# Kernel tuning notes

Measured on AMD Instinct MI355X. Metric: run time of the kernel, lower is better.

The kernel has to match this reference:

```python
import jax, jax.numpy as jnp
import numpy as np

N = 50000
IN_DIM = 128
HID = 16
HEADS = 8
NUM_CLASSES = 16
NEG_SLOPE = 0.2


def _glorot(key, shape):
    fan_in, fan_out = shape[0], shape[-1]
    lim = float(np.sqrt(6.0 / (fan_in + fan_out)))
    return jax.random.uniform(key, shape, jnp.float32, -lim, lim)


def setup_inputs() -> dict:
    key = jax.random.key(0)
    ks = jax.random.split(key, 12)
    x = jax.random.normal(ks[0], (N, IN_DIM), jnp.float32)
    edge_index = jax.random.randint(ks[1], (2, 1600000), 0, N, jnp.int64)
    # conv1: in=IN_DIM, out per head=HID, heads=HEADS
    Wl1 = _glorot(ks[2], (IN_DIM, HEADS * HID))
    Wr1 = _glorot(ks[3], (IN_DIM, HEADS * HID))
    att1 = _glorot(ks[4], (HEADS, HID))
    b1 = jnp.zeros((HEADS * HID,), jnp.float32)
    # conv2: in=HID*HEADS, out per head=NUM_CLASSES
    Wl2 = _glorot(ks[5], (HEADS * HID, HEADS * NUM_CLASSES))
    Wr2 = _glorot(ks[6], (HEADS * HID, HEADS * NUM_CLASSES))
    att2 = _glorot(ks[7], (HEADS, NUM_CLASSES))
    b2 = jnp.zeros((HEADS * NUM_CLASSES,), jnp.float32)
    # final linear: NUM_CLASSES*HEADS -> NUM_CLASSES
    Wlin = _glorot(ks[8], (HEADS * NUM_CLASSES, NUM_CLASSES))
    blin = jnp.zeros((NUM_CLASSES,), jnp.float32)
    return dict(x=x, edge_index=edge_index, Wl1=Wl1, Wr1=Wr1, att1=att1, b1=b1,
                Wl2=Wl2, Wr2=Wr2, att2=att2, b2=b2, Wlin=Wlin, blin=blin)


def _gatv2_conv(x, src, dst, Wl, Wr, att, bias, heads, out_ch):
    n = x.shape[0]
    xl = (x @ Wl).reshape(n, heads, out_ch)  # source transform
    xr = (x @ Wr).reshape(n, heads, out_ch)  # target transform
    # additive attention logits per edge (GATv2)
    e = jax.nn.leaky_relu(xl[src] + xr[dst], NEG_SLOPE)          # [E,H,C]
    logits = jnp.einsum('ehc,hc->eh', e, att)                     # [E,H]
    # per-destination segment softmax
    m = jax.ops.segment_max(logits, dst, num_segments=n)          # [N,H]
    a = jnp.exp(logits - m[dst])                                  # [E,H]
    s = jax.ops.segment_sum(a, dst, num_segments=n)               # [N,H]
    alpha = a / (s[dst] + 1e-16)
    out = jax.ops.segment_sum(alpha[:, :, None] * xl[src], dst, num_segments=n)
    return out.reshape(n, heads * out_ch) + bias


def reference(x, edge_index, Wl1, Wr1, att1, b1, Wl2, Wr2, att2, b2, Wlin, blin):
    n = x.shape[0]
    # add self-loops (PyG GATv2Conv default add_self_loops=True)
    loop = jnp.arange(n, dtype=edge_index.dtype)
    src = jnp.concatenate([edge_index[0], loop])
    dst = jnp.concatenate([edge_index[1], loop])
    h = _gatv2_conv(x, src, dst, Wl1, Wr1, att1, b1, HEADS, HID)
    h = jax.nn.relu(h)  # dropout identity in eval mode
    h = _gatv2_conv(h, src, dst, Wl2, Wr2, att2, b2, HEADS, NUM_CLASSES)
    h = jax.nn.relu(h)
    logits = h @ Wlin + blin
    return jax.nn.log_softmax(logits, axis=1)
```

## Files before the change

kernel.cpp:

```cpp
#include <hip/hip_runtime.h>

#define HEADS 8
#define FDIM 128
#define NCLS 16
#define NEG_SLOPE 0.2f
#define LOG2E 1.4426950408889634f

typedef __attribute__((ext_vector_type(8))) short bf16x8;
typedef __attribute__((ext_vector_type(4))) float f32x4;

__device__ __forceinline__ unsigned short f2bf(float f) {
    unsigned u = __float_as_uint(f);
    unsigned r = u + 0x7FFFu + ((u >> 16) & 1u);
    return (unsigned short)(r >> 16);
}

__global__ __launch_bounds__(256) void gemm_csr(const float* __restrict__ Xf,
                                                const unsigned short* __restrict__ Xb,
                                                const float* __restrict__ W0,
                                                const float* __restrict__ W1,
                                                unsigned short* __restrict__ Y0,
                                                unsigned short* __restrict__ Y1,
                                                int n,
                                                const int* __restrict__ srcs,
                                                const int* __restrict__ dsts,
                                                int* __restrict__ cnt,
                                                int* __restrict__ adj,
                                                int E0, int pad, int GB, int SB) {
    __shared__ __align__(16) unsigned short ws[8 * 4 * 64 * 8];
    const int t = threadIdx.x;
    const int x = blockIdx.x;
    if (x >= 2 * GB) {
        int i = (x - 2 * GB) * 256 + t;
        const int stride = SB * 256;
        for (; i < E0; i += stride) {
            const int d = dsts[i];
            const int rk = atomicAdd(&cnt[d], 1);
            if (rk < pad) adj[(size_t)d * pad + rk] = srcs[i];
        }
        return;
    }
    const int side = (x >= GB) ? 1 : 0;
    const float* W = side ? W1 : W0;
    unsigned short* Y = side ? Y1 : Y0;

#pragma unroll
    for (int i = 0; i < 16; i++) {
        const int f = t + i * 256;
        const int k = f >> 5, n4 = f & 31;
        const float4 v = *(const float4*)(W + k * 128 + n4 * 4);
        const int kc = k >> 5, q = (k >> 3) & 3, j = k & 7;
        const float vv[4] = {v.x, v.y, v.z, v.w};
#pragma unroll
        for (int e = 0; e < 4; e++) {
            const int nn = n4 * 4 + e;
            ws[((((nn >> 4) * 4 + kc) * 64 + q * 16 + (nn & 15)) << 3) + j] = f2bf(vv[e]);
        }
    }
    __syncthreads();

    const int w = t >> 6, lane = t & 63;
    const int q = lane >> 4, m = lane & 15;
    const bf16x8* wb = (const bf16x8*)ws;
    const int Gh = (n + 63) >> 6;
    const int bid = side ? x - GB : x;

    for (int tile = bid; tile < Gh; tile += GB) {
        const int nb = tile * 64;
        const int arow = nb + w * 16 + m;
        bf16x8 af[4];
        if (arow < n) {
            if (Xb) {
                const unsigned short* xp = Xb + (size_t)arow * 128 + q * 8;
#pragma unroll
                for (int kc = 0; kc < 4; kc++) af[kc] = *(const bf16x8*)(xp + kc * 32);
            } else {
                const float* xp = Xf + (size_t)arow * 128 + q * 8;
#pragma unroll
                for (int kc = 0; kc < 4; kc++) {
                    const float4 v0 = *(const float4*)(xp + kc * 32);
                    const float4 v1 = *(const float4*)(xp + kc * 32 + 4);
                    union { unsigned short us[8]; bf16x8 b; } pk;
                    pk.us[0] = f2bf(v0.x); pk.us[1] = f2bf(v0.y);
                    pk.us[2] = f2bf(v0.z); pk.us[3] = f2bf(v0.w);
                    pk.us[4] = f2bf(v1.x); pk.us[5] = f2bf(v1.y);
                    pk.us[6] = f2bf(v1.z); pk.us[7] = f2bf(v1.w);
                    af[kc] = pk.b;
                }
            }
        } else {
#pragma unroll
            for (int kc = 0; kc < 4; kc++) af[kc] = (bf16x8){0,0,0,0,0,0,0,0};
        }
        f32x4 acc[8];
#pragma unroll
        for (int i = 0; i < 8; i++) acc[i] = (f32x4){0.f, 0.f, 0.f, 0.f};
#pragma unroll
        for (int kc = 0; kc < 4; kc++) {
#pragma unroll
            for (int ct = 0; ct < 8; ct++)
                acc[ct] = __builtin_amdgcn_mfma_f32_16x16x32_bf16(
                    af[kc], wb[(ct * 4 + kc) * 64 + lane], acc[ct], 0, 0, 0);
        }
#pragma unroll
        for (int ct = 0; ct < 8; ct++) {
#pragma unroll
            for (int r = 0; r < 4; r++) {
                const int row = nb + w * 16 + q * 4 + r;
                if (row < n) Y[(size_t)row * 128 + ct * 16 + m] = f2bf(acc[ct][r]);
            }
        }
    }
}

#define GATHER_EDGE(pA, pB, S_, A0_, A1_, A2_, A3_)                          \
    {                                                                        \
        const int src_ = half ? (pB) : (pA);                                 \
        const uint2 lv_ = *(const uint2*)(xl + (size_t)src_ * FDIM + col);   \
        const float l0_ = __uint_as_float(lv_.x << 16);                      \
        const float l1_ = __uint_as_float(lv_.x & 0xFFFF0000u);              \
        const float l2_ = __uint_as_float(lv_.y << 16);                      \
        const float l3_ = __uint_as_float(lv_.y & 0xFFFF0000u);              \
        float z0_ = l0_ + r0; z0_ = fmaxf(z0_, NEG_SLOPE * z0_);             \
        float z1_ = l1_ + r1; z1_ = fmaxf(z1_, NEG_SLOPE * z1_);             \
        float z2_ = l2_ + r2; z2_ = fmaxf(z2_, NEG_SLOPE * z2_);             \
        float z3_ = l3_ + r3; z3_ = fmaxf(z3_, NEG_SLOPE * z3_);             \
        float p_ = z0_ * a0 + z1_ * a1 + z2_ * a2 + z3_ * a3;                \
        p_ += __shfl_xor(p_, 1, 64);                                         \
        p_ += __shfl_xor(p_, 2, 64);                                         \
        const float e_ = exp2f(p_ - mx);                                     \
        S_ += e_;                                                            \
        A0_ += e_ * l0_; A1_ += e_ * l1_; A2_ += e_ * l2_; A3_ += e_ * l3_;  \
    }

__global__ __launch_bounds__(256) void node_gather(const unsigned short* __restrict__ xl,
                                                   const unsigned short* __restrict__ xr,
                                                   const float* __restrict__ att,
                                                   const int* __restrict__ adj,
                                                   const int* __restrict__ cnt,
                                                   const float* __restrict__ bias,
                                                   unsigned short* __restrict__ outC,
                                                   const float* __restrict__ headW,
                                                   const float* __restrict__ headB,
                                                   float* __restrict__ outH,
                                                   int n, int pad) {
    __shared__ float WsL[FDIM * NCLS];
    __shared__ __align__(16) float stage[4][FDIM];
    const int t = threadIdx.x;
    if (headW) {
        for (int i = t; i < FDIM * NCLS; i += 256) WsL[i] = headW[i];
        __syncthreads();
    }
    const int lane = t & 63;
    const int w = t >> 6;
    const int node = blockIdx.x * 4 + w;
    if (node >= n) return;
    const int half = lane >> 5;
    const int sub = lane & 31;
    const int col = sub * 4;
    const float4 av = *(const float4*)(att + col);
    const float a0 = av.x * LOG2E, a1 = av.y * LOG2E;
    const float a2 = av.z * LOG2E, a3 = av.w * LOG2E;

    float r0, r1, r2, r3, sl0, sl1, sl2, sl3;
    {
        const uint2 rv = *(const uint2*)(xr + (size_t)node * FDIM + col);
        r0 = __uint_as_float(rv.x << 16); r1 = __uint_as_float(rv.x & 0xFFFF0000u);
        r2 = __uint_as_float(rv.y << 16); r3 = __uint_as_float(rv.y & 0xFFFF0000u);
        const uint2 lv = *(const uint2*)(xl + (size_t)node * FDIM + col);
        sl0 = __uint_as_float(lv.x << 16); sl1 = __uint_as_float(lv.x & 0xFFFF0000u);
        sl2 = __uint_as_float(lv.y << 16); sl3 = __uint_as_float(lv.y & 0xFFFF0000u);
    }
    float mx;
    {
        float z0 = sl0 + r0; z0 = fmaxf(z0, NEG_SLOPE * z0);
        float z1 = sl1 + r1; z1 = fmaxf(z1, NEG_SLOPE * z1);
        float z2 = sl2 + r2; z2 = fmaxf(z2, NEG_SLOPE * z2);
        float z3 = sl3 + r3; z3 = fmaxf(z3, NEG_SLOPE * z3);
        float p = z0 * a0 + z1 * a1 + z2 * a2 + z3 * a3;
        p += __shfl_xor(p, 1, 64);
        p += __shfl_xor(p, 2, 64);
        mx = p;
    }
    float sA, aA0, aA1, aA2, aA3;
    float sB = 0.f, aB0 = 0.f, aB1 = 0.f, aB2 = 0.f, aB3 = 0.f;
    if (half == 0) { sA = 1.f; aA0 = sl0; aA1 = sl1; aA2 = sl2; aA3 = sl3; }
    else           { sA = 0.f; aA0 = aA1 = aA2 = aA3 = 0.f; }

    const int* ap = adj + (size_t)node * pad;
    const int deg = min(cnt[node], pad);
    int j = 0;
    for (; j + 8 <= deg; j += 8) {
        const int4 sa = *(const int4*)(ap + j);
        const int4 sb = *(const int4*)(ap + j + 4);
        GATHER_EDGE(sa.x, sa.y, sA, aA0, aA1, aA2, aA3)
        GATHER_EDGE(sa.z, sa.w, sB, aB0, aB1, aB2, aB3)
        GATHER_EDGE(sb.x, sb.y, sA, aA0, aA1, aA2, aA3)
        GATHER_EDGE(sb.z, sb.w, sB, aB0, aB1, aB2, aB3)
    }
    for (; j < deg; j += 2) {
        const int pA = ap[j];
        const int pB = (j + 1 < deg) ? ap[j + 1] : pA;
        const float gate = (half == 0 || j + 1 < deg) ? 1.f : 0.f;
        const int src = half ? pB : pA;
        const uint2 lv = *(const uint2*)(xl + (size_t)src * FDIM + col);
        const float l0 = __uint_as_float(lv.x << 16);
        const float l1 = __uint_as_float(lv.x & 0xFFFF0000u);
        const float l2 = __uint_as_float(lv.y << 16);
        const float l3 = __uint_as_float(lv.y & 0xFFFF0000u);
        float z0 = l0 + r0; z0 = fmaxf(z0, NEG_SLOPE * z0);
        float z1 = l1 + r1; z1 = fmaxf(z1, NEG_SLOPE * z1);
        float z2 = l2 + r2; z2 = fmaxf(z2, NEG_SLOPE * z2);
        float z3 = l3 + r3; z3 = fmaxf(z3, NEG_SLOPE * z3);
        float p = z0 * a0 + z1 * a1 + z2 * a2 + z3 * a3;
        p += __shfl_xor(p, 1, 64);
        p += __shfl_xor(p, 2, 64);
        const float e = exp2f(p - mx) * gate;
        sA += e;
        aA0 += e * l0; aA1 += e * l1; aA2 += e * l2; aA3 += e * l3;
    }
    float s = sA + sB;
    float acc0 = aA0 + aB0, acc1 = aA1 + aB1, acc2 = aA2 + aB2, acc3 = aA3 + aB3;
    s    += __shfl_xor(s, 32, 64);
    acc0 += __shfl_xor(acc0, 32, 64);
    acc1 += __shfl_xor(acc1, 32, 64);
    acc2 += __shfl_xor(acc2, 32, 64);
    acc3 += __shfl_xor(acc3, 32, 64);

    const float inv = 1.f / (s + 1e-16f);
    const float4 bv = *(const float4*)(bias + col);
    const float o0 = fmaxf(acc0 * inv + bv.x, 0.f);
    const float o1 = fmaxf(acc1 * inv + bv.y, 0.f);
    const float o2 = fmaxf(acc2 * inv + bv.z, 0.f);
    const float o3 = fmaxf(acc3 * inv + bv.w, 0.f);

    if (!headW) {
        if (half == 0) {
            union { unsigned short us[4]; uint2 u2; } pk;
            pk.us[0] = f2bf(o0); pk.us[1] = f2bf(o1);
            pk.us[2] = f2bf(o2); pk.us[3] = f2bf(o3);
            *(uint2*)(outC + (size_t)node * FDIM + col) = pk.u2;
        }
        return;
    }
    if (half == 0)
        *(float4*)&stage[w][col] = make_float4(o0, o1, o2, o3);
    const int cls = lane & 15;
    const int q = lane >> 4;
    float acc = 0.f;
#pragma unroll
    for (int k = 0; k < 32; k++)
        acc += stage[w][q * 32 + k] * WsL[(q * 32 + k) * NCLS + cls];
    acc += __shfl_xor(acc, 16, 64);
    acc += __shfl_xor(acc, 32, 64);
    acc += headB[cls];
    float m2 = acc;
    m2 = fmaxf(m2, __shfl_xor(m2, 8, 64));
    m2 = fmaxf(m2, __shfl_xor(m2, 4, 64));
    m2 = fmaxf(m2, __shfl_xor(m2, 2, 64));
    m2 = fmaxf(m2, __shfl_xor(m2, 1, 64));
    float sm = __expf(acc - m2);
    sm += __shfl_xor(sm, 8, 64);
    sm += __shfl_xor(sm, 4, 64);
    sm += __shfl_xor(sm, 2, 64);
    sm += __shfl_xor(sm, 1, 64);
    if (lane < 16)
        outH[(size_t)node * NCLS + cls] = acc - m2 - __logf(sm);
}

extern "C" void kernel_launch(void* const* d_in, const int* in_sizes, int n_in,
                              void* d_out, int out_size, void* d_ws, size_t ws_size,
                              hipStream_t stream) {
    const float* x    = (const float*)d_in[0];
    const int*   edge = (const int*)d_in[1];
    const float* Wl1  = (const float*)d_in[2];
    const float* Wr1  = (const float*)d_in[3];
    const float* att1 = (const float*)d_in[4];
    const float* b1   = (const float*)d_in[5];
    const float* Wl2  = (const float*)d_in[6];
    const float* Wr2  = (const float*)d_in[7];
    const float* att2 = (const float*)d_in[8];
    const float* b2   = (const float*)d_in[9];
    const float* Wlin = (const float*)d_in[10];
    const float* blin = (const float*)d_in[11];

    const int N = in_sizes[0] / FDIM;
    const int E0 = in_sizes[1] / 2;
    const int* srcs = edge;
    const int* dsts = edge + E0;

    int PAD = 96;
    {
        size_t need = (size_t)3 * N * FDIM * 2 + (size_t)N * 4 + (size_t)N * PAD * 4;
        if (need > ws_size) PAD = 72;
    }

    unsigned short* A = (unsigned short*)d_ws;
    unsigned short* B = A + (size_t)N * FDIM;
    unsigned short* C = B + (size_t)N * FDIM;
    int* cnt   = (int*)(C + (size_t)N * FDIM);
    int* adj   = cnt + N;

    const int GB = 320;
    const int SB = 256;
    const int node_blocks = (N + 3) / 4;

    hipMemsetAsync(cnt, 0, (size_t)N * sizeof(int), stream);

    gemm_csr<<<2 * GB + SB, 256, 0, stream>>>(
        x, nullptr, Wl1, Wr1, A, B, N, srcs, dsts, cnt, adj, E0, PAD, GB, SB);
    node_gather<<<node_blocks, 256, 0, stream>>>(A, B, att1, adj, cnt, b1, C,
                                                 nullptr, nullptr, nullptr, N, PAD);

    gemm_csr<<<2 * GB, 256, 0, stream>>>(
        nullptr, C, Wl2, Wr2, A, B, N, nullptr, nullptr, nullptr, nullptr, 0, PAD, GB, 0);
    node_gather<<<node_blocks, 256, 0, stream>>>(A, B, att2, adj, cnt, b2,
                                                 nullptr, Wlin, blin,
                                                 (float*)d_out, N, PAD);
}
```

Before: 394.8 us.

## Gather four edges per wavefront with 16-lane groups and 16-byte loads

```diff
diff --git a/kernel.cpp b/kernel.cpp
--- a/kernel.cpp
+++ b/kernel.cpp
@@ -113,26 +113,34 @@
     }
 }
 
-#define GATHER_EDGE(pA, pB, S_, A0_, A1_, A2_, A3_)                          \
+#define GATHER_EDGE4(SRC, GATE)                                              \
     {                                                                        \
-        const int src_ = half ? (pB) : (pA);                                 \
-        const uint2 lv_ = *(const uint2*)(xl + (size_t)src_ * FDIM + col);   \
+        const uint4 lv_ = *(const uint4*)(xl + (size_t)(SRC) * FDIM + col);  \
         const float l0_ = __uint_as_float(lv_.x << 16);                      \
         const float l1_ = __uint_as_float(lv_.x & 0xFFFF0000u);              \
         const float l2_ = __uint_as_float(lv_.y << 16);                      \
         const float l3_ = __uint_as_float(lv_.y & 0xFFFF0000u);              \
-        float z0_ = l0_ + r0; z0_ = fmaxf(z0_, NEG_SLOPE * z0_);             \
-        float z1_ = l1_ + r1; z1_ = fmaxf(z1_, NEG_SLOPE * z1_);             \
-        float z2_ = l2_ + r2; z2_ = fmaxf(z2_, NEG_SLOPE * z2_);             \
-        float z3_ = l3_ + r3; z3_ = fmaxf(z3_, NEG_SLOPE * z3_);             \
-        float p_ = z0_ * a0 + z1_ * a1 + z2_ * a2 + z3_ * a3;                \
+        const float l4_ = __uint_as_float(lv_.z << 16);                      \
+        const float l5_ = __uint_as_float(lv_.z & 0xFFFF0000u);              \
+        const float l6_ = __uint_as_float(lv_.w << 16);                      \
+        const float l7_ = __uint_as_float(lv_.w & 0xFFFF0000u);              \
+        float z_, p_;                                                        \
+        z_ = l0_ + r0; z_ = fmaxf(z_, NEG_SLOPE * z_); p_  = z_ * a0;        \
+        z_ = l1_ + r1; z_ = fmaxf(z_, NEG_SLOPE * z_); p_ += z_ * a1;        \
+        z_ = l2_ + r2; z_ = fmaxf(z_, NEG_SLOPE * z_); p_ += z_ * a2;        \
+        z_ = l3_ + r3; z_ = fmaxf(z_, NEG_SLOPE * z_); p_ += z_ * a3;        \
+        z_ = l4_ + r4; z_ = fmaxf(z_, NEG_SLOPE * z_); p_ += z_ * a4;        \
+        z_ = l5_ + r5; z_ = fmaxf(z_, NEG_SLOPE * z_); p_ += z_ * a5;        \
+        z_ = l6_ + r6; z_ = fmaxf(z_, NEG_SLOPE * z_); p_ += z_ * a6;        \
+        z_ = l7_ + r7; z_ = fmaxf(z_, NEG_SLOPE * z_); p_ += z_ * a7;        \
         p_ += __shfl_xor(p_, 1, 64);                                         \
-        p_ += __shfl_xor(p_, 2, 64);                                         \
-        const float e_ = exp2f(p_ - mx);                                     \
-        S_ += e_;                                                            \
-        A0_ += e_ * l0_; A1_ += e_ * l1_; A2_ += e_ * l2_; A3_ += e_ * l3_;  \
-    }
-
+        const float e_ = exp2f(p_ - mx) * (GATE);                            \
+        s += e_;                                                             \
+        c0 += e_ * l0_; c1 += e_ * l1_; c2 += e_ * l2_; c3 += e_ * l3_;      \
+        c4 += e_ * l4_; c5 += e_ * l5_; c6 += e_ * l6_; c7 += e_ * l7_;      \
+    }
+
+template <bool HEAD>
 __global__ __launch_bounds__(256) void node_gather(const unsigned short* __restrict__ xl,
                                                    const unsigned short* __restrict__ xr,
                                                    const float* __restrict__ att,
@@ -144,10 +152,10 @@
                                                    const float* __restrict__ headB,
                                                    float* __restrict__ outH,
                                                    int n, int pad) {
-    __shared__ float WsL[FDIM * NCLS];
-    __shared__ __align__(16) float stage[4][FDIM];
+    __shared__ float WsL[HEAD ? FDIM * NCLS : 1];
+    __shared__ __align__(16) float stage[HEAD ? 4 : 1][FDIM];
     const int t = threadIdx.x;
-    if (headW) {
+    if (HEAD) {
         for (int i = t; i < FDIM * NCLS; i += 256) WsL[i] = headW[i];
         __syncthreads();
     }
@@ -155,96 +163,100 @@
     const int w = t >> 6;
     const int node = blockIdx.x * 4 + w;
     if (node >= n) return;
-    const int half = lane >> 5;
-    const int sub = lane & 31;
-    const int col = sub * 4;
-    const float4 av = *(const float4*)(att + col);
-    const float a0 = av.x * LOG2E, a1 = av.y * LOG2E;
-    const float a2 = av.z * LOG2E, a3 = av.w * LOG2E;
-
-    float r0, r1, r2, r3, sl0, sl1, sl2, sl3;
-    {
-        const uint2 rv = *(const uint2*)(xr + (size_t)node * FDIM + col);
+    const int g = lane >> 4;
+    const int sub = lane & 15;
+    const int col = sub * 8;
+    float a0, a1, a2, a3, a4, a5, a6, a7;
+    {
+        const float4 v0 = *(const float4*)(att + col);
+        const float4 v1 = *(const float4*)(att + col + 4);
+        a0 = v0.x * LOG2E; a1 = v0.y * LOG2E; a2 = v0.z * LOG2E; a3 = v0.w * LOG2E;
+        a4 = v1.x * LOG2E; a5 = v1.y * LOG2E; a6 = v1.z * LOG2E; a7 = v1.w * LOG2E;
+    }
+    float r0, r1, r2, r3, r4, r5, r6, r7;
+    float sl0, sl1, sl2, sl3, sl4, sl5, sl6, sl7;
+    {
+        const uint4 rv = *(const uint4*)(xr + (size_t)node * FDIM + col);
         r0 = __uint_as_float(rv.x << 16); r1 = __uint_as_float(rv.x & 0xFFFF0000u);
         r2 = __uint_as_float(rv.y << 16); r3 = __uint_as_float(rv.y & 0xFFFF0000u);
-        const uint2 lv = *(const uint2*)(xl + (size_t)node * FDIM + col);
+        r4 = __uint_as_float(rv.z << 16); r5 = __uint_as_float(rv.z & 0xFFFF0000u);
+        r6 = __uint_as_float(rv.w << 16); r7 = __uint_as_float(rv.w & 0xFFFF0000u);
+        const uint4 lv = *(const uint4*)(xl + (size_t)node * FDIM + col);
         sl0 = __uint_as_float(lv.x << 16); sl1 = __uint_as_float(lv.x & 0xFFFF0000u);
         sl2 = __uint_as_float(lv.y << 16); sl3 = __uint_as_float(lv.y & 0xFFFF0000u);
+        sl4 = __uint_as_float(lv.z << 16); sl5 = __uint_as_float(lv.z & 0xFFFF0000u);
+        sl6 = __uint_as_float(lv.w << 16); sl7 = __uint_as_float(lv.w & 0xFFFF0000u);
     }
     float mx;
     {
-        float z0 = sl0 + r0; z0 = fmaxf(z0, NEG_SLOPE * z0);
-        float z1 = sl1 + r1; z1 = fmaxf(z1, NEG_SLOPE * z1);
-        float z2 = sl2 + r2; z2 = fmaxf(z2, NEG_SLOPE * z2);
-        float z3 = sl3 + r3; z3 = fmaxf(z3, NEG_SLOPE * z3);
-        float p = z0 * a0 + z1 * a1 + z2 * a2 + z3 * a3;
+        float z, p;
+        z = sl0 + r0; z = fmaxf(z, NEG_SLOPE * z); p  = z * a0;
+        z = sl1 + r1; z = fmaxf(z, NEG_SLOPE * z); p += z * a1;
+        z = sl2 + r2; z = fmaxf(z, NEG_SLOPE * z); p += z * a2;
+        z = sl3 + r3; z = fmaxf(z, NEG_SLOPE * z); p += z * a3;
+        z = sl4 + r4; z = fmaxf(z, NEG_SLOPE * z); p += z * a4;
+        z = sl5 + r5; z = fmaxf(z, NEG_SLOPE * z); p += z * a5;
+        z = sl6 + r6; z = fmaxf(z, NEG_SLOPE * z); p += z * a6;
+        z = sl7 + r7; z = fmaxf(z, NEG_SLOPE * z); p += z * a7;
         p += __shfl_xor(p, 1, 64);
-        p += __shfl_xor(p, 2, 64);
         mx = p;
     }
-    float sA, aA0, aA1, aA2, aA3;
-    float sB = 0.f, aB0 = 0.f, aB1 = 0.f, aB2 = 0.f, aB3 = 0.f;
-    if (half == 0) { sA = 1.f; aA0 = sl0; aA1 = sl1; aA2 = sl2; aA3 = sl3; }
-    else           { sA = 0.f; aA0 = aA1 = aA2 = aA3 = 0.f; }
+    float s, c0, c1, c2, c3, c4, c5, c6, c7;
+    if (g == 0) { s = 1.f; c0 = sl0; c1 = sl1; c2 = sl2; c3 = sl3;
+                  c4 = sl4; c5 = sl5; c6 = sl6; c7 = sl7; }
+    else        { s = 0.f; c0 = c1 = c2 = c3 = c4 = c5 = c6 = c7 = 0.f; }
 
     const int* ap = adj + (size_t)node * pad;
     const int deg = min(cnt[node], pad);
     int j = 0;
     for (; j + 8 <= deg; j += 8) {
-        const int4 sa = *(const int4*)(ap + j);
-        const int4 sb = *(const int4*)(ap + j + 4);
-        GATHER_EDGE(sa.x, sa.y, sA, aA0, aA1, aA2, aA3)
-        GATHER_EDGE(sa.z, sa.w, sB, aB0, aB1, aB2, aB3)
-        GATHER_EDGE(sb.x, sb.y, sA, aA0, aA1, aA2, aA3)
-        GATHER_EDGE(sb.z, sb.w, sB, aB0, aB1, aB2, aB3)
-    }
-    for (; j < deg; j += 2) {
-        const int pA = ap[j];
-        const int pB = (j + 1 < deg) ? ap[j + 1] : pA;
-        const float gate = (half == 0 || j + 1 < deg) ? 1.f : 0.f;
-        const int src = half ? pB : pA;
-        const uint2 lv = *(const uint2*)(xl + (size_t)src * FDIM + col);
-        const float l0 = __uint_as_float(lv.x << 16);
-        const float l1 = __uint_as_float(lv.x & 0xFFFF0000u);
-        const float l2 = __uint_as_float(lv.y << 16);
-        const float l3 = __uint_as_float(lv.y & 0xFFFF0000u);
-        float z0 = l0 + r0; z0 = fmaxf(z0, NEG_SLOPE * z0);
-        float z1 = l1 + r1; z1 = fmaxf(z1, NEG_SLOPE * z1);
-        float z2 = l2 + r2; z2 = fmaxf(z2, NEG_SLOPE * z2);
-        float z3 = l3 + r3; z3 = fmaxf(z3, NEG_SLOPE * z3);
-        float p = z0 * a0 + z1 * a1 + z2 * a2 + z3 * a3;
-        p += __shfl_xor(p, 1, 64);
-        p += __shfl_xor(p, 2, 64);
-        const float e = exp2f(p - mx) * gate;
-        sA += e;
-        aA0 += e * l0; aA1 += e * l1; aA2 += e * l2; aA3 += e * l3;
-    }
-    float s = sA + sB;
-    float acc0 = aA0 + aB0, acc1 = aA1 + aB1, acc2 = aA2 + aB2, acc3 = aA3 + aB3;
-    s    += __shfl_xor(s, 32, 64);
-    acc0 += __shfl_xor(acc0, 32, 64);
-    acc1 += __shfl_xor(acc1, 32, 64);
-    acc2 += __shfl_xor(acc2, 32, 64);
-    acc3 += __shfl_xor(acc3, 32, 64);
+        const int e0 = ap[j + g];
+        const int e1 = ap[j + 4 + g];
+        GATHER_EDGE4(e0, 1.f)
+        GATHER_EDGE4(e1, 1.f)
+    }
+    for (; j < deg; j += 4) {
+        const int idx = j + g;
+        const int e0 = (idx < deg) ? ap[idx] : ap[deg - 1];
+        const float gate = (idx < deg) ? 1.f : 0.f;
+        GATHER_EDGE4(e0, gate)
+    }
+    s  += __shfl_xor(s, 16, 64);  s  += __shfl_xor(s, 32, 64);
+    c0 += __shfl_xor(c0, 16, 64); c0 += __shfl_xor(c0, 32, 64);
+    c1 += __shfl_xor(c1, 16, 64); c1 += __shfl_xor(c1, 32, 64);
+    c2 += __shfl_xor(c2, 16, 64); c2 += __shfl_xor(c2, 32, 64);
+    c3 += __shfl_xor(c3, 16, 64); c3 += __shfl_xor(c3, 32, 64);
+    c4 += __shfl_xor(c4, 16, 64); c4 += __shfl_xor(c4, 32, 64);
+    c5 += __shfl_xor(c5, 16, 64); c5 += __shfl_xor(c5, 32, 64);
+    c6 += __shfl_xor(c6, 16, 64); c6 += __shfl_xor(c6, 32, 64);
+    c7 += __shfl_xor(c7, 16, 64); c7 += __shfl_xor(c7, 32, 64);
 
     const float inv = 1.f / (s + 1e-16f);
-    const float4 bv = *(const float4*)(bias + col);
-    const float o0 = fmaxf(acc0 * inv + bv.x, 0.f);
-    const float o1 = fmaxf(acc1 * inv + bv.y, 0.f);
-    const float o2 = fmaxf(acc2 * inv + bv.z, 0.f);
-    const float o3 = fmaxf(acc3 * inv + bv.w, 0.f);
-
-    if (!headW) {
-        if (half == 0) {
-            union { unsigned short us[4]; uint2 u2; } pk;
+    float o0, o1, o2, o3, o4, o5, o6, o7;
+    {
+        const float4 b0 = *(const float4*)(bias + col);
+        const float4 b1 = *(const float4*)(bias + col + 4);
+        o0 = fmaxf(c0 * inv + b0.x, 0.f); o1 = fmaxf(c1 * inv + b0.y, 0.f);
+        o2 = fmaxf(c2 * inv + b0.z, 0.f); o3 = fmaxf(c3 * inv + b0.w, 0.f);
+        o4 = fmaxf(c4 * inv + b1.x, 0.f); o5 = fmaxf(c5 * inv + b1.y, 0.f);
+        o6 = fmaxf(c6 * inv + b1.z, 0.f); o7 = fmaxf(c7 * inv + b1.w, 0.f);
+    }
+
+    if (!HEAD) {
+        if (g == 0) {
+            union { unsigned short us[8]; uint4 u4; } pk;
             pk.us[0] = f2bf(o0); pk.us[1] = f2bf(o1);
             pk.us[2] = f2bf(o2); pk.us[3] = f2bf(o3);
-            *(uint2*)(outC + (size_t)node * FDIM + col) = pk.u2;
+            pk.us[4] = f2bf(o4); pk.us[5] = f2bf(o5);
+            pk.us[6] = f2bf(o6); pk.us[7] = f2bf(o7);
+            *(uint4*)(outC + (size_t)node * FDIM + col) = pk.u4;
         }
         return;
     }
-    if (half == 0)
-        *(float4*)&stage[w][col] = make_float4(o0, o1, o2, o3);
+    if (g == 0) {
+        *(float4*)&stage[w][col]     = make_float4(o0, o1, o2, o3);
+        *(float4*)&stage[w][col + 4] = make_float4(o4, o5, o6, o7);
+    }
     const int cls = lane & 15;
     const int q = lane >> 4;
     float acc = 0.f;
@@ -309,12 +321,11 @@
 
     gemm_csr<<<2 * GB + SB, 256, 0, stream>>>(
         x, nullptr, Wl1, Wr1, A, B, N, srcs, dsts, cnt, adj, E0, PAD, GB, SB);
-    node_gather<<<node_blocks, 256, 0, stream>>>(A, B, att1, adj, cnt, b1, C,
-                                                 nullptr, nullptr, nullptr, N, PAD);
+    node_gather<false><<<node_blocks, 256, 0, stream>>>(
+        A, B, att1, adj, cnt, b1, C, nullptr, nullptr, nullptr, N, PAD);
 
     gemm_csr<<<2 * GB, 256, 0, stream>>>(
         nullptr, C, Wl2, Wr2, A, B, N, nullptr, nullptr, nullptr, nullptr, 0, PAD, GB, 0);
-    node_gather<<<node_blocks, 256, 0, stream>>>(A, B, att2, adj, cnt, b2,
-                                                 nullptr, Wlin, blin,
-                                                 (float*)d_out, N, PAD);
+    node_gather<true><<<node_blocks, 256, 0, stream>>>(
+        A, B, att2, adj, cnt, b2, nullptr, Wlin, blin, (float*)d_out, N, PAD);
 }
```

Result: faster. 364.1 us (-7.8%).
